# Kernel tuning notes

Measured on AMD Instinct MI355X. Metric: run time of the kernel, lower is better.

Reference implementation:

```python
import jax, jax.numpy as jnp
import numpy as np

N_HEAD = 12
LN_EPS = 1e-5


def setup_inputs() -> dict:
    key = jax.random.key(0)
    ks = jax.random.split(key, 4)
    B, T, C = 4, 2048, 768
    s = C ** -0.5
    return {
        "x": jax.random.normal(ks[0], (B, T, C), jnp.float32),
        "w_attn": jax.random.normal(ks[1], (C, 3 * C), jnp.float32) * s,
        "b_attn": jnp.zeros((3 * C,), jnp.float32),
        "w_proj": jax.random.normal(ks[2], (C, C), jnp.float32) * s,
        "b_proj": jnp.zeros((C,), jnp.float32),
        "ln1_g": jnp.ones((C,), jnp.float32),
        "ln1_b": jnp.zeros((C,), jnp.float32),
        "ln2_g": jnp.ones((C,), jnp.float32),
        "ln2_b": jnp.zeros((C,), jnp.float32),
    }


def _layernorm(x, g, b):
    mu = jnp.mean(x, axis=-1, keepdims=True)
    var = jnp.mean(jnp.square(x - mu), axis=-1, keepdims=True)
    return (x - mu) * jax.lax.rsqrt(var + LN_EPS) * g + b


def _attn(h, w_attn, b_attn, w_proj, b_proj):
    B, T, C = h.shape
    hd = C // N_HEAD
    # Faithful to torch: view(B,T,H,3*hd) then split 3*hd -> q,k,v per head
    qkv = (h @ w_attn + b_attn).reshape(B, T, N_HEAD, 3, hd)
    q = jnp.transpose(qkv[:, :, :, 0, :], (0, 2, 1, 3))  # (B,H,T,hd)
    k = jnp.transpose(qkv[:, :, :, 1, :], (0, 2, 1, 3))
    v = jnp.transpose(qkv[:, :, :, 2, :], (0, 2, 1, 3))
    # NOTE: scale is C**-0.5 (full embed dim) and there is NO causal mask,
    # exactly as in the source.
    scores = jnp.einsum("bhtd,bhsd->bhts", q, k) * (C ** -0.5)
    a = jax.nn.softmax(scores, axis=-1)
    y = jnp.einsum("bhts,bhsd->bhtd", a, v)
    y = jnp.transpose(y, (0, 2, 1, 3)).reshape(B, T, C)
    return y @ w_proj + b_proj


def reference(x, w_attn, b_attn, w_proj, b_proj, ln1_g, ln1_b, ln2_g, ln2_b):
    # Faithful to source Block.forward: attn applied twice, MLP never called.
    x = x + _attn(_layernorm(x, ln1_g, ln1_b), w_attn, b_attn, w_proj, b_proj)
    x = x + _attn(_layernorm(x, ln2_g, ln2_b), w_attn, b_attn, w_proj, b_proj)
    return x
```

## Files before the change

### kernel.cpp

```cpp
#include <hip/hip_runtime.h>


using bf16x8 = __attribute__((ext_vector_type(8))) short;
using f32x4  = __attribute__((ext_vector_type(4))) float;

__device__ __forceinline__ unsigned short f2b(float f) {
  unsigned u = __builtin_bit_cast(unsigned, f);
  u += 0x7FFFu + ((u >> 16) & 1u);
  return (unsigned short)(u >> 16);
}

#define ASYNC16(g, l)                                                        \
  __builtin_amdgcn_global_load_lds(                                          \
      (const __attribute__((address_space(1))) void*)(g),                    \
      (__attribute__((address_space(3))) void*)(l), 16, 0, 0)

__global__ __launch_bounds__(256) void wt_kernel(const float* __restrict__ w,
                                                 unsigned short* __restrict__ wt,
                                                 int N) {
  __shared__ float tile[32][33];
  const int n0 = blockIdx.x * 32, k0 = blockIdx.y * 32;
  const int tx = threadIdx.x, ty = threadIdx.y;
#pragma unroll
  for (int i = 0; i < 32; i += 8)
    tile[ty + i][tx] = w[(size_t)(k0 + ty + i) * N + n0 + tx];
  __syncthreads();
#pragma unroll
  for (int i = 0; i < 32; i += 8)
    wt[(size_t)(n0 + ty + i) * 768 + k0 + tx] = f2b(tile[tx][ty + i]);
}

__global__ __launch_bounds__(256) void ln_kernel(const float* __restrict__ x,
                                                 const float* __restrict__ g,
                                                 const float* __restrict__ b,
                                                 unsigned short* __restrict__ h) {
  __shared__ float red[8];
  const int row = blockIdx.x;
  const int tid = threadIdx.x;
  const float* xr = x + (size_t)row * 768;
  float v0 = xr[tid], v1 = xr[tid + 256], v2 = xr[tid + 512];
  float s = v0 + v1 + v2;
  float s2 = v0 * v0 + v1 * v1 + v2 * v2;
#pragma unroll
  for (int off = 1; off < 64; off <<= 1) {
    s += __shfl_xor(s, off);
    s2 += __shfl_xor(s2, off);
  }
  if ((tid & 63) == 0) { red[tid >> 6] = s; red[4 + (tid >> 6)] = s2; }
  __syncthreads();
  const float S  = red[0] + red[1] + red[2] + red[3];
  const float S2 = red[4] + red[5] + red[6] + red[7];
  const float mu  = S * (1.0f / 768.0f);
  const float var = S2 * (1.0f / 768.0f) - mu * mu;
  const float inv = rsqrtf(var + 1e-5f);
  unsigned short* hr = h + (size_t)row * 768;
  hr[tid]       = f2b((v0 - mu) * inv * g[tid] + b[tid]);
  hr[tid + 256] = f2b((v1 - mu) * inv * g[tid + 256] + b[tid + 256]);
  hr[tid + 512] = f2b((v2 - mu) * inv * g[tid + 512] + b[tid + 512]);
}

template <int EPI>
__global__ __launch_bounds__(256, 2) void gemm_kernel(
    const unsigned short* __restrict__ A, const unsigned short* __restrict__ Bt,
    const float* __restrict__ bias, const float* __restrict__ resid,
    unsigned short* __restrict__ q, unsigned short* __restrict__ k,
    unsigned short* __restrict__ v, float* __restrict__ outF) {
  __shared__ alignas(16) unsigned short As[128 * 32];
  __shared__ alignas(16) unsigned short Bs[128 * 32];

  const int tid = threadIdx.x;
  const int wv = tid >> 6;
  const int lane = tid & 63;
  const int quad = lane >> 4;
  const int l15 = lane & 15;
  const int m0 = blockIdx.y * 128;
  const int n0 = blockIdx.x * 128;

  const int o0 = wv * 1024 + lane * 16;
  const int rT0 = o0 >> 6, c0 = (o0 & 63) >> 1;
  const int o1 = o0 + 4096;
  const int rT1 = o1 >> 6, c1 = (o1 & 63) >> 1;

  const unsigned short* gA0 = A + (size_t)(m0 + rT0) * 768 + c0;
  const unsigned short* gA1 = A + (size_t)(m0 + rT1) * 768 + c1;
  const unsigned short* gB0 = Bt + (size_t)(n0 + rT0) * 768 + c0;
  const unsigned short* gB1 = Bt + (size_t)(n0 + rT1) * 768 + c1;
  unsigned short* lA0 = &As[wv * 512];
  unsigned short* lA1 = &As[wv * 512 + 2048];
  unsigned short* lB0 = &Bs[wv * 512];
  unsigned short* lB1 = &Bs[wv * 512 + 2048];

  f32x4 acc[4][4];
#pragma unroll
  for (int i = 0; i < 4; ++i)
#pragma unroll
    for (int j = 0; j < 4; ++j) acc[i][j] = {0.f, 0.f, 0.f, 0.f};

  const int mBase = (wv >> 1) * 64;
  const int nBase = (wv & 1) * 64;

  for (int kk = 0; kk < 24; ++kk) {
    const int ko = kk * 32;
    ASYNC16(gA0 + ko, lA0);
    ASYNC16(gA1 + ko, lA1);
    ASYNC16(gB0 + ko, lB0);
    ASYNC16(gB1 + ko, lB1);
    __syncthreads();
    bf16x8 af[4], bfv[4];
#pragma unroll
    for (int mt = 0; mt < 4; ++mt)
      af[mt] = *(const bf16x8*)&As[(mBase + mt * 16 + l15) * 32 + quad * 8];
#pragma unroll
    for (int nt = 0; nt < 4; ++nt)
      bfv[nt] = *(const bf16x8*)&Bs[(nBase + nt * 16 + l15) * 32 + quad * 8];
#pragma unroll
    for (int mt = 0; mt < 4; ++mt)
#pragma unroll
      for (int nt = 0; nt < 4; ++nt)
        acc[mt][nt] = __builtin_amdgcn_mfma_f32_16x16x32_bf16(af[mt], bfv[nt],
                                                              acc[mt][nt], 0, 0, 0);
    __syncthreads();
  }

  if constexpr (EPI == 0) {
#pragma unroll
    for (int mt = 0; mt < 4; ++mt) {
#pragma unroll
      for (int nt = 0; nt < 4; ++nt) {
        const int n = n0 + nBase + nt * 16 + l15;
        const int head = n / 192;
        const int rem = n - head * 192;
        const int sel = rem >> 6;
        const int d = rem & 63;
        unsigned short* tgt = (sel == 0) ? q : (sel == 1) ? k : v;
        const float bv = bias[n];
#pragma unroll
        for (int r = 0; r < 4; ++r) {
          const int m = m0 + mBase + mt * 16 + quad * 4 + r;
          const int bb = m >> 11;
          const int t = m & 2047;
          tgt[(((size_t)bb * 12 + head) * 2048 + t) * 64 + d] =
              f2b(acc[mt][nt][r] + bv);
        }
      }
    }
  } else {
#pragma unroll
    for (int mt = 0; mt < 4; ++mt) {
#pragma unroll
      for (int nt = 0; nt < 4; ++nt) {
        const int n = n0 + nBase + nt * 16 + l15;
        const float bv = bias[n];
#pragma unroll
        for (int r = 0; r < 4; ++r) {
          const int m = m0 + mBase + mt * 16 + quad * 4 + r;
          const size_t idx = (size_t)m * 768 + n;
          outF[idx] = resid[idx] + bv + acc[mt][nt][r];
        }
      }
    }
  }
}

__global__ __launch_bounds__(256) void vtrans_kernel(const unsigned short* __restrict__ V,
                                                     unsigned short* __restrict__ Vt) {
  const int bh = blockIdx.x;
  const int t = blockIdx.y * 256 + threadIdx.x;
  const uint4* s4 = (const uint4*)(V + ((size_t)bh * 2048 + t) * 64);
  const size_t ob = (size_t)bh * 64 * 2048 + t;
#pragma unroll
  for (int i = 0; i < 8; ++i) {
    const uint4 u = s4[i];
    const unsigned w[4] = {u.x, u.y, u.z, u.w};
#pragma unroll
    for (int j = 0; j < 4; ++j) {
      Vt[ob + (size_t)(i * 8 + j * 2) * 2048]     = (unsigned short)(w[j] & 0xFFFFu);
      Vt[ob + (size_t)(i * 8 + j * 2 + 1) * 2048] = (unsigned short)(w[j] >> 16);
    }
  }
}

#define PAD 68
__global__ __launch_bounds__(256, 3) void attn_kernel(
    const unsigned short* __restrict__ Q, const unsigned short* __restrict__ Km,
    const unsigned short* __restrict__ Vt, unsigned short* __restrict__ Y) {
  __shared__ alignas(16) unsigned short Ks[64 * PAD];
  __shared__ alignas(16) unsigned short Vs[64 * PAD];
  __shared__ alignas(16) unsigned short Ps[4][32 * PAD];

  const int bh = blockIdx.x;
  const int qt = blockIdx.y;
  const int tid = threadIdx.x;
  const int wv = tid >> 6;
  const int lane = tid & 63;
  const int quad = lane >> 4;
  const int l15 = lane & 15;
  const size_t bhT = (size_t)bh * 2048;

  bf16x8 qf[2][2];
#pragma unroll
  for (int mt = 0; mt < 2; ++mt) {
    const unsigned short* qb = Q + (bhT + qt * 128 + mt * 64 + wv * 16 + l15) * 64;
    qf[mt][0] = *(const bf16x8*)(qb + quad * 8);
    qf[mt][1] = *(const bf16x8*)(qb + 32 + quad * 8);
  }

  f32x4 o[2][4], ol[2];
#pragma unroll
  for (int mt = 0; mt < 2; ++mt) {
    ol[mt] = {0.f, 0.f, 0.f, 0.f};
#pragma unroll
    for (int nt = 0; nt < 4; ++nt) o[mt][nt] = {0.f, 0.f, 0.f, 0.f};
  }
  const bf16x8 ones = {0x3F80, 0x3F80, 0x3F80, 0x3F80,
                       0x3F80, 0x3F80, 0x3F80, 0x3F80};

  const int kr = tid >> 3;
  const int kc = (tid & 7) * 8;
  const unsigned short* gK = Km + (bhT + kr) * 64 + kc;
  const unsigned short* gV = Vt + ((size_t)bh * 64 + kr) * 2048 + kc;
  unsigned short* lK0 = &Ks[kr * PAD + kc];
  unsigned short* lK1 = &Ks[(kr + 32) * PAD + kc];
  unsigned short* lV0 = &Vs[kr * PAD + kc];
  unsigned short* lV1 = &Vs[(kr + 32) * PAD + kc];
  const float c2 = 0.052062786090587f;

  bf16x8 sk0 = *(const bf16x8*)(gK);
  bf16x8 sk1 = *(const bf16x8*)(gK + 32 * 64);
  bf16x8 sv0 = *(const bf16x8*)(gV);
  bf16x8 sv1 = *(const bf16x8*)(gV + 32 * 2048);

  for (int c = 0; c < 32; ++c) {
    *(bf16x8*)lK0 = sk0;
    *(bf16x8*)lK1 = sk1;
    *(bf16x8*)lV0 = sv0;
    *(bf16x8*)lV1 = sv1;
    __syncthreads();
    if (c < 31) {
      sk0 = *(const bf16x8*)(gK + (size_t)(c + 1) * 4096);
      sk1 = *(const bf16x8*)(gK + (size_t)(c + 1) * 4096 + 2048);
      sv0 = *(const bf16x8*)(gV + (c + 1) * 64);
      sv1 = *(const bf16x8*)(gV + (c + 1) * 64 + 32 * 2048);
    }

    f32x4 s[2][4];
#pragma unroll
    for (int nt = 0; nt < 4; ++nt) {
      s[0][nt] = {0.f, 0.f, 0.f, 0.f};
      s[1][nt] = {0.f, 0.f, 0.f, 0.f};
#pragma unroll
      for (int ks = 0; ks < 2; ++ks) {
        bf16x8 kf = *(const bf16x8*)&Ks[(nt * 16 + l15) * PAD + ks * 32 + quad * 8];
        s[0][nt] = __builtin_amdgcn_mfma_f32_16x16x32_bf16(qf[0][ks], kf, s[0][nt], 0, 0, 0);
        s[1][nt] = __builtin_amdgcn_mfma_f32_16x16x32_bf16(qf[1][ks], kf, s[1][nt], 0, 0, 0);
      }
    }

#pragma unroll
    for (int mt = 0; mt < 2; ++mt)
#pragma unroll
      for (int nt = 0; nt < 4; ++nt)
#pragma unroll
        for (int r = 0; r < 4; ++r) {
          const float p = __builtin_amdgcn_exp2f(s[mt][nt][r] * c2);
          Ps[wv][(mt * 16 + quad * 4 + r) * PAD + nt * 16 + l15] =
              (unsigned short)(__builtin_bit_cast(unsigned, p) >> 16);
        }

#pragma unroll
    for (int ks = 0; ks < 2; ++ks) {
      bf16x8 pf0 = *(const bf16x8*)&Ps[wv][(l15) * PAD + ks * 32 + quad * 8];
      bf16x8 pf1 = *(const bf16x8*)&Ps[wv][(16 + l15) * PAD + ks * 32 + quad * 8];
      ol[0] = __builtin_amdgcn_mfma_f32_16x16x32_bf16(pf0, ones, ol[0], 0, 0, 0);
      ol[1] = __builtin_amdgcn_mfma_f32_16x16x32_bf16(pf1, ones, ol[1], 0, 0, 0);
#pragma unroll
      for (int nt = 0; nt < 4; ++nt) {
        bf16x8 vf = *(const bf16x8*)&Vs[(nt * 16 + l15) * PAD + ks * 32 + quad * 8];
        o[0][nt] = __builtin_amdgcn_mfma_f32_16x16x32_bf16(pf0, vf, o[0][nt], 0, 0, 0);
        o[1][nt] = __builtin_amdgcn_mfma_f32_16x16x32_bf16(pf1, vf, o[1][nt], 0, 0, 0);
      }
    }
    __syncthreads();
  }

  const int b = bh / 12;
  const int head = bh - b * 12;
#pragma unroll
  for (int mt = 0; mt < 2; ++mt) {
    const int qrow0 = qt * 128 + mt * 64 + wv * 16 + quad * 4;
#pragma unroll
    for (int r = 0; r < 4; ++r) {
      const float rl = 1.0f / ol[mt][r];
#pragma unroll
      for (int nt = 0; nt < 4; ++nt)
        Y[((size_t)(b * 2048 + qrow0 + r)) * 768 + head * 64 + nt * 16 + l15] =
            f2b(o[mt][nt][r] * rl);
    }
  }
}

extern "C" void kernel_launch(void* const* d_in, const int* in_sizes, int n_in,
                              void* d_out, int out_size, void* d_ws, size_t ws_size,
                              hipStream_t stream) {
  const float* x      = (const float*)d_in[0];
  const float* w_attn = (const float*)d_in[1];
  const float* b_attn = (const float*)d_in[2];
  const float* w_proj = (const float*)d_in[3];
  const float* b_proj = (const float*)d_in[4];
  const float* ln_g[2] = {(const float*)d_in[5], (const float*)d_in[7]};
  const float* ln_b[2] = {(const float*)d_in[6], (const float*)d_in[8]};
  float* out = (float*)d_out;

  unsigned short* wAt = (unsigned short*)d_ws;
  unsigned short* wPt = wAt + 2304 * 768;
  unsigned short* h   = wPt + 768 * 768;
  unsigned short* q   = h + 8192 * 768;
  unsigned short* k   = q + 48 * 2048 * 64;
  unsigned short* v   = k + 48 * 2048 * 64;
  unsigned short* vt  = v + 48 * 2048 * 64;
  unsigned short* y   = vt + 48 * 2048 * 64;

  wt_kernel<<<dim3(72, 24), dim3(32, 8), 0, stream>>>(w_attn, wAt, 2304);
  wt_kernel<<<dim3(24, 24), dim3(32, 8), 0, stream>>>(w_proj, wPt, 768);

  for (int pass = 0; pass < 2; ++pass) {
    const float* xin = pass ? (const float*)out : x;
    ln_kernel<<<8192, 256, 0, stream>>>(xin, ln_g[pass], ln_b[pass], h);
    gemm_kernel<0><<<dim3(18, 64), 256, 0, stream>>>(h, wAt, b_attn, nullptr,
                                                     q, k, v, nullptr);
    vtrans_kernel<<<dim3(48, 8), 256, 0, stream>>>(v, vt);
    attn_kernel<<<dim3(48, 16), 256, 0, stream>>>(q, k, vt, y);
    gemm_kernel<1><<<dim3(6, 64), 256, 0, stream>>>(y, wPt, b_proj, xin,
                                                    nullptr, nullptr, nullptr, out);
  }
}
```

Before: 439.6 us.

## Split attention over key range, fuse V transpose into QKV GEMM epilogue

Removes the separate V-transpose kernel by having the QKV GEMM epilogue write V directly in transposed layout. The attention kernel is split into two halves over the key sequence (grid z=2), each writing unnormalized bf16 partial outputs and row sums. A new combine kernel adds the halves and normalizes. Occupancy hint is raised to 4 blocks per SIMD group. The aim is more blocks in flight for a 768-block grid, at the cost of extra partial-output traffic and a bf16 rounding of the partial sums. This works without a max-subtraction step because the code already relies on fixed-scale exponentials.

```diff
diff --git a/kernel.cpp b/kernel.cpp
--- a/kernel.cpp
+++ b/kernel.cpp
@@ -8,6 +8,9 @@
   unsigned u = __builtin_bit_cast(unsigned, f);
   u += 0x7FFFu + ((u >> 16) & 1u);
   return (unsigned short)(u >> 16);
+}
+__device__ __forceinline__ float b2f(unsigned short s) {
+  return __builtin_bit_cast(float, (unsigned)s << 16);
 }
 
 #define ASYNC16(g, l)                                                        \
@@ -64,7 +67,7 @@
     const unsigned short* __restrict__ A, const unsigned short* __restrict__ Bt,
     const float* __restrict__ bias, const float* __restrict__ resid,
     unsigned short* __restrict__ q, unsigned short* __restrict__ k,
-    unsigned short* __restrict__ v, float* __restrict__ outF) {
+    unsigned short* __restrict__ vt, float* __restrict__ outF) {
   __shared__ alignas(16) unsigned short As[128 * 32];
   __shared__ alignas(16) unsigned short Bs[128 * 32];
 
@@ -132,15 +135,19 @@
         const int rem = n - head * 192;
         const int sel = rem >> 6;
         const int d = rem & 63;
-        unsigned short* tgt = (sel == 0) ? q : (sel == 1) ? k : v;
         const float bv = bias[n];
 #pragma unroll
         for (int r = 0; r < 4; ++r) {
           const int m = m0 + mBase + mt * 16 + quad * 4 + r;
           const int bb = m >> 11;
           const int t = m & 2047;
-          tgt[(((size_t)bb * 12 + head) * 2048 + t) * 64 + d] =
-              f2b(acc[mt][nt][r] + bv);
+          const unsigned short val = f2b(acc[mt][nt][r] + bv);
+          if (sel == 2) {
+            vt[(((size_t)bb * 12 + head) * 64 + d) * 2048 + t] = val;
+          } else {
+            unsigned short* tgt = (sel == 0) ? q : k;
+            tgt[(((size_t)bb * 12 + head) * 2048 + t) * 64 + d] = val;
+          }
         }
       }
     }
@@ -162,34 +169,18 @@
   }
 }
 
-__global__ __launch_bounds__(256) void vtrans_kernel(const unsigned short* __restrict__ V,
-                                                     unsigned short* __restrict__ Vt) {
-  const int bh = blockIdx.x;
-  const int t = blockIdx.y * 256 + threadIdx.x;
-  const uint4* s4 = (const uint4*)(V + ((size_t)bh * 2048 + t) * 64);
-  const size_t ob = (size_t)bh * 64 * 2048 + t;
-#pragma unroll
-  for (int i = 0; i < 8; ++i) {
-    const uint4 u = s4[i];
-    const unsigned w[4] = {u.x, u.y, u.z, u.w};
-#pragma unroll
-    for (int j = 0; j < 4; ++j) {
-      Vt[ob + (size_t)(i * 8 + j * 2) * 2048]     = (unsigned short)(w[j] & 0xFFFFu);
-      Vt[ob + (size_t)(i * 8 + j * 2 + 1) * 2048] = (unsigned short)(w[j] >> 16);
-    }
-  }
-}
-
 #define PAD 68
-__global__ __launch_bounds__(256, 3) void attn_kernel(
+__global__ __launch_bounds__(256, 4) void attn_kernel(
     const unsigned short* __restrict__ Q, const unsigned short* __restrict__ Km,
-    const unsigned short* __restrict__ Vt, unsigned short* __restrict__ Y) {
+    const unsigned short* __restrict__ Vt, unsigned short* __restrict__ Opart,
+    float* __restrict__ lpart) {
   __shared__ alignas(16) unsigned short Ks[64 * PAD];
   __shared__ alignas(16) unsigned short Vs[64 * PAD];
   __shared__ alignas(16) unsigned short Ps[4][32 * PAD];
 
   const int bh = blockIdx.x;
   const int qt = blockIdx.y;
+  const int split = blockIdx.z;
   const int tid = threadIdx.x;
   const int wv = tid >> 6;
   const int lane = tid & 63;
@@ -225,18 +216,19 @@
   unsigned short* lV1 = &Vs[(kr + 32) * PAD + kc];
   const float c2 = 0.052062786090587f;
 
-  bf16x8 sk0 = *(const bf16x8*)(gK);
-  bf16x8 sk1 = *(const bf16x8*)(gK + 32 * 64);
-  bf16x8 sv0 = *(const bf16x8*)(gV);
-  bf16x8 sv1 = *(const bf16x8*)(gV + 32 * 2048);
-
-  for (int c = 0; c < 32; ++c) {
+  const int cBeg = split * 16, cEnd = cBeg + 16;
+  bf16x8 sk0 = *(const bf16x8*)(gK + (size_t)cBeg * 4096);
+  bf16x8 sk1 = *(const bf16x8*)(gK + (size_t)cBeg * 4096 + 2048);
+  bf16x8 sv0 = *(const bf16x8*)(gV + cBeg * 64);
+  bf16x8 sv1 = *(const bf16x8*)(gV + cBeg * 64 + 32 * 2048);
+
+  for (int c = cBeg; c < cEnd; ++c) {
     *(bf16x8*)lK0 = sk0;
     *(bf16x8*)lK1 = sk1;
     *(bf16x8*)lV0 = sv0;
     *(bf16x8*)lV1 = sv1;
     __syncthreads();
-    if (c < 31) {
+    if (c + 1 < cEnd) {
       sk0 = *(const bf16x8*)(gK + (size_t)(c + 1) * 4096);
       sk1 = *(const bf16x8*)(gK + (size_t)(c + 1) * 4096 + 2048);
       sv0 = *(const bf16x8*)(gV + (c + 1) * 64);
@@ -283,19 +275,44 @@
     __syncthreads();
   }
 
+  unsigned short* Ob = Opart + ((size_t)split * 48 + bh) * 2048 * 64;
+  float* lb = lpart + ((size_t)split * 48 + bh) * 2048;
+#pragma unroll
+  for (int mt = 0; mt < 2; ++mt) {
+#pragma unroll
+    for (int r = 0; r < 4; ++r) {
+      const int t = qt * 128 + mt * 64 + wv * 16 + quad * 4 + r;
+#pragma unroll
+      for (int nt = 0; nt < 4; ++nt)
+        Ob[(size_t)t * 64 + nt * 16 + l15] = f2b(o[mt][nt][r]);
+      if (l15 == 0) lb[t] = ol[mt][r];
+    }
+  }
+}
+
+__global__ __launch_bounds__(256) void combine_kernel(
+    const unsigned short* __restrict__ Opart, const float* __restrict__ lpart,
+    unsigned short* __restrict__ Y) {
+  const int bh = blockIdx.x;
+  const int t = blockIdx.y * 256 + threadIdx.x;
   const int b = bh / 12;
   const int head = bh - b * 12;
-#pragma unroll
-  for (int mt = 0; mt < 2; ++mt) {
-    const int qrow0 = qt * 128 + mt * 64 + wv * 16 + quad * 4;
-#pragma unroll
-    for (int r = 0; r < 4; ++r) {
-      const float rl = 1.0f / ol[mt][r];
-#pragma unroll
-      for (int nt = 0; nt < 4; ++nt)
-        Y[((size_t)(b * 2048 + qrow0 + r)) * 768 + head * 64 + nt * 16 + l15] =
-            f2b(o[mt][nt][r] * rl);
-    }
+  const size_t i0 = ((size_t)bh * 2048 + t) * 64;
+  const size_t i1 = ((size_t)(48 + bh) * 2048 + t) * 64;
+  const float l = lpart[(size_t)bh * 2048 + t] + lpart[(size_t)(48 + bh) * 2048 + t];
+  const float rl = 1.0f / l;
+  unsigned short* yb = Y + ((size_t)(b * 2048 + t)) * 768 + head * 64;
+#pragma unroll
+  for (int j = 0; j < 8; ++j) {
+    bf16x8 a = *(const bf16x8*)(Opart + i0 + j * 8);
+    bf16x8 c = *(const bf16x8*)(Opart + i1 + j * 8);
+    bf16x8 r;
+#pragma unroll
+    for (int e = 0; e < 8; ++e) {
+      const float v = (b2f((unsigned short)a[e]) + b2f((unsigned short)c[e])) * rl;
+      r[e] = (short)f2b(v);
+    }
+    *(bf16x8*)(yb + j * 8) = r;
   }
 }
 
@@ -316,9 +333,10 @@
   unsigned short* h   = wPt + 768 * 768;
   unsigned short* q   = h + 8192 * 768;
   unsigned short* k   = q + 48 * 2048 * 64;
-  unsigned short* v   = k + 48 * 2048 * 64;
-  unsigned short* vt  = v + 48 * 2048 * 64;
+  unsigned short* vt  = k + 48 * 2048 * 64;
   unsigned short* y   = vt + 48 * 2048 * 64;
+  unsigned short* Op  = y + 8192 * 768;
+  float* lp = (float*)(Op + 2 * 48 * 2048 * 64);
 
   wt_kernel<<<dim3(72, 24), dim3(32, 8), 0, stream>>>(w_attn, wAt, 2304);
   wt_kernel<<<dim3(24, 24), dim3(32, 8), 0, stream>>>(w_proj, wPt, 768);
@@ -327,9 +345,9 @@
     const float* xin = pass ? (const float*)out : x;
     ln_kernel<<<8192, 256, 0, stream>>>(xin, ln_g[pass], ln_b[pass], h);
     gemm_kernel<0><<<dim3(18, 64), 256, 0, stream>>>(h, wAt, b_attn, nullptr,
-                                                     q, k, v, nullptr);
-    vtrans_kernel<<<dim3(48, 8), 256, 0, stream>>>(v, vt);
-    attn_kernel<<<dim3(48, 16), 256, 0, stream>>>(q, k, vt, y);
+                                                     q, k, vt, nullptr);
+    attn_kernel<<<dim3(48, 16, 2), 256, 0, stream>>>(q, k, vt, Op, lp);
+    combine_kernel<<<dim3(48, 8), 256, 0, stream>>>(Op, lp, y);
     gemm_kernel<1><<<dim3(6, 64), 256, 0, stream>>>(y, wPt, b_proj, xin,
                                                     nullptr, nullptr, nullptr, out);
   }
```

Measured after the change: 467.6 us. +6.4%, slower.
